# Kernel tuning notes

Measured on AMD Instinct MI355X. Metric: run time of the kernel, lower is better.

The kernel has to match this reference:

```python
import jax, jax.numpy as jnp
import numpy as np

NUM_TOKENS = 8192
CODEBOOK_DIM = 64
BETA = 0.25
DECAY = 0.99
EPS = 1e-05
B, C, H, W = 32, 64, 32, 32


def setup_inputs() -> dict:
    key = jax.random.key(0)
    k1, k2, k3, k4 = jax.random.split(key, 4)
    z = jax.random.normal(k1, (B, C, H, W), dtype=jnp.float32)
    emb = jax.random.normal(k2, (NUM_TOKENS, CODEBOOK_DIM), dtype=jnp.float32)
    ema_w = jax.random.normal(k3, (NUM_TOKENS, CODEBOOK_DIM), dtype=jnp.float32)
    cluster_size = jax.random.uniform(k4, (NUM_TOKENS,), dtype=jnp.float32)
    return {"z": z, "emb": emb, "ema_w": ema_w, "cluster_size": cluster_size}


def reference(z, emb, ema_w, cluster_size):
    # NCHW -> NHWC, flatten to [N, D]
    z_nhwc = jnp.transpose(z, (0, 2, 3, 1))
    z_flat = z_nhwc.reshape(-1, CODEBOOK_DIM)  # [N, D]

    # squared distances: ||z||^2 + ||e||^2 - 2 z e^T  -> [N, K]
    d = (jnp.sum(z_flat * z_flat, axis=1, keepdims=True)
         + jnp.sum(emb * emb, axis=1)
         - 2.0 * jnp.einsum('nd,kd->nk', z_flat, emb))
    idx = jnp.argmin(d, axis=1)  # [N] int

    z_q = emb[idx].reshape(z_nhwc.shape)  # gather + reshape

    # EMA updates (training-mode buffer math); one-hot matmuls expressed as segment sums
    new_cluster = jax.ops.segment_sum(jnp.ones_like(idx, dtype=z.dtype), idx, num_segments=NUM_TOKENS)
    cs = DECAY * cluster_size + (1.0 - DECAY) * new_cluster
    new_ema_w = jax.ops.segment_sum(z_flat, idx, num_segments=NUM_TOKENS)
    ema_w_out = DECAY * ema_w + (1.0 - DECAY) * new_ema_w
    cs_sum = jnp.sum(cs)
    cs_norm = (cs + EPS) / (cs_sum + NUM_TOKENS * EPS)
    emb_out = ema_w_out / cs_norm[:, None]

    # commitment loss uses z_q from the OLD codebook (as in torch code)
    loss = BETA * jnp.mean((jax.lax.stop_gradient(z_q) - z_nhwc) ** 2)

    # straight-through estimator, back to NCHW
    z_q_st = z_nhwc + jax.lax.stop_gradient(z_q - z_nhwc)
    z_q_st = jnp.transpose(z_q_st, (0, 3, 1, 2))
    return z_q_st, loss, idx, cs_norm, ema_w_out, emb_out
```

## Files before the change

### kernel.cpp

```cpp
#include <hip/hip_runtime.h>
#include <float.h>

#define N_TOK   32768
#define DIM     64
#define K_CODES 8192
#define HWSZ    1024
#define CHW     65536
#define NELEM   2097152

typedef short  bf16x8 __attribute__((ext_vector_type(8)));
typedef float  f32x16 __attribute__((ext_vector_type(16)));

static __device__ __forceinline__ unsigned short f2bf(float x) {
    unsigned u = __float_as_uint(x);
    unsigned r = u + 0x7FFFu + ((u >> 16) & 1u);
    return (unsigned short)(r >> 16);
}
static __device__ __forceinline__ float bf2f(unsigned short h) {
    return __uint_as_float(((unsigned)h) << 16);
}

__global__ __launch_bounds__(256) void prep_e(const float* __restrict__ emb,
                                              unsigned short* __restrict__ blob,
                                              float* __restrict__ eng,
                                              unsigned long long* __restrict__ packed,
                                              int* __restrict__ cnt_i,
                                              float* __restrict__ sums) {
    __shared__ float part[512];
    const int gid = blockIdx.x * 256 + threadIdx.x;
    packed[gid] = ~0ull;
    if (gid < K_CODES) cnt_i[gid] = 0;
    if (gid < 2) sums[gid] = 0.f;

    int tile = blockIdx.x;
    #pragma unroll
    for (int u0 = 0; u0 < 2; ++u0) {
        int u = threadIdx.x + u0 * 256;
        int s = u >> 7, h = (u >> 6) & 1, n = u & 63;
        const float* src = emb + (tile * 64 + n) * 64 + s * 16 + h * 8;
        float4 v0 = *(const float4*)src;
        float4 v1 = *(const float4*)(src + 4);
        float x[8] = {v0.x, v0.y, v0.z, v0.w, v1.x, v1.y, v1.z, v1.w};
        unsigned short hi[8], lo[8];
        float ss = 0.f;
        #pragma unroll
        for (int j = 0; j < 8; ++j) {
            hi[j] = f2bf(x[j]);
            lo[j] = f2bf(x[j] - bf2f(hi[j]));
            ss += x[j] * x[j];
        }
        part[u] = ss;
        unsigned short* dhi = blob + (size_t)tile * 8192 + ((s * 2 + 0) * 2 + h) * 512 + n * 8;
        unsigned short* dlo = blob + (size_t)tile * 8192 + ((s * 2 + 1) * 2 + h) * 512 + n * 8;
        uint4 ph, pl;
        ph.x = (unsigned)hi[0] | ((unsigned)hi[1] << 16);
        ph.y = (unsigned)hi[2] | ((unsigned)hi[3] << 16);
        ph.z = (unsigned)hi[4] | ((unsigned)hi[5] << 16);
        ph.w = (unsigned)hi[6] | ((unsigned)hi[7] << 16);
        pl.x = (unsigned)lo[0] | ((unsigned)lo[1] << 16);
        pl.y = (unsigned)lo[2] | ((unsigned)lo[3] << 16);
        pl.z = (unsigned)lo[4] | ((unsigned)lo[5] << 16);
        pl.w = (unsigned)lo[6] | ((unsigned)lo[7] << 16);
        *(uint4*)dhi = ph;
        *(uint4*)dlo = pl;
    }
    __syncthreads();
    if (threadIdx.x < 64) {
        float s = 0.f;
        #pragma unroll
        for (int j = 0; j < 8; ++j) s += part[threadIdx.x + j * 64];
        eng[tile * 64 + threadIdx.x] = s;
    }
}

__global__ __launch_bounds__(256, 3) void vq_argmin(const float* __restrict__ z,
                                                    const unsigned short* __restrict__ blob,
                                                    const float* __restrict__ eng,
                                                    unsigned long long* __restrict__ packed) {
    __shared__ __align__(16) unsigned short zh[64 * 72];
    __shared__ __align__(16) unsigned short zl[64 * 72];
    __shared__ unsigned long long red[64 * 4];

    const int tid  = threadIdx.x;
    const int lane = tid & 63;
    const int wid  = tid >> 6;
    const int l31  = lane & 31, h = lane >> 5;

    const int tb = blockIdx.x & 511;
    const int ks = blockIdx.x >> 9;
    const int n0 = tb * 64;
    const int zbase = (n0 >> 10) * CHW + (n0 & 1023);

    {
        int f4 = tid & 15;
        int c0 = tid >> 4;
        #pragma unroll
        for (int r = 0; r < 4; ++r) {
            int c = c0 * 4 + r;
            float4 v = *(const float4*)(z + zbase + c * HWSZ + f4 * 4);
            float x[4] = {v.x, v.y, v.z, v.w};
            #pragma unroll
            for (int e = 0; e < 4; ++e) {
                int t = f4 * 4 + e;
                float xs = -2.0f * x[e];
                unsigned short hi = f2bf(xs);
                zh[t * 72 + c] = hi;
                zl[t * 72 + c] = f2bf(xs - bf2f(hi));
            }
        }
    }
    __syncthreads();

    bf16x8 T0h[4], T0l[4], T1h[4], T1l[4];
    {
        int r0 = l31;
        int r1 = 32 + l31;
        #pragma unroll
        for (int s = 0; s < 4; ++s) {
            T0h[s] = *(const bf16x8*)(&zh[r0 * 72 + s * 16 + h * 8]);
            T0l[s] = *(const bf16x8*)(&zl[r0 * 72 + s * 16 + h * 8]);
            T1h[s] = *(const bf16x8*)(&zh[r1 * 72 + s * 16 + h * 8]);
            T1l[s] = *(const bf16x8*)(&zl[r1 * 72 + s * 16 + h * 8]);
        }
    }

    float minv0 = FLT_MAX, minv1 = FLT_MAX;
    int   mini0 = 0,       mini1 = 0;

    const int hk0 = ks * 128 + wid, hk1 = ks * 128 + 128;
    for (int hk = hk0; hk < hk1; hk += 4) {
        bf16x8 Eh[4], El[4];
        const unsigned short* base = blob + (size_t)(hk >> 1) * 8192 + ((hk & 1) * 32 + l31) * 8;
        #pragma unroll
        for (int s = 0; s < 4; ++s) {
            Eh[s] = *(const bf16x8*)(base + (4 * s + h) * 512);
            El[s] = *(const bf16x8*)(base + (4 * s + 2 + h) * 512);
        }
        const int cb = (hk >> 1) * 64 + (hk & 1) * 32 + 4 * h;
        const float* ebase = eng + cb;
        float4 e0 = *(const float4*)(ebase);
        float4 e1 = *(const float4*)(ebase + 8);
        float4 e2 = *(const float4*)(ebase + 16);
        float4 e3 = *(const float4*)(ebase + 24);
        f32x16 ac0, ac1;
        ac0[0]  = e0.x; ac0[1]  = e0.y; ac0[2]  = e0.z; ac0[3]  = e0.w;
        ac0[4]  = e1.x; ac0[5]  = e1.y; ac0[6]  = e1.z; ac0[7]  = e1.w;
        ac0[8]  = e2.x; ac0[9]  = e2.y; ac0[10] = e2.z; ac0[11] = e2.w;
        ac0[12] = e3.x; ac0[13] = e3.y; ac0[14] = e3.z; ac0[15] = e3.w;
        ac1 = ac0;
        #pragma unroll
        for (int s = 0; s < 4; ++s) {
            ac0 = __builtin_amdgcn_mfma_f32_32x32x16_bf16(El[s], T0h[s], ac0, 0, 0, 0);
            ac1 = __builtin_amdgcn_mfma_f32_32x32x16_bf16(El[s], T1h[s], ac1, 0, 0, 0);
            ac0 = __builtin_amdgcn_mfma_f32_32x32x16_bf16(Eh[s], T0l[s], ac0, 0, 0, 0);
            ac1 = __builtin_amdgcn_mfma_f32_32x32x16_bf16(Eh[s], T1l[s], ac1, 0, 0, 0);
            ac0 = __builtin_amdgcn_mfma_f32_32x32x16_bf16(Eh[s], T0h[s], ac0, 0, 0, 0);
            ac1 = __builtin_amdgcn_mfma_f32_32x32x16_bf16(Eh[s], T1h[s], ac1, 0, 0, 0);
        }
        #pragma unroll
        for (int r = 0; r < 16; ++r) {
            int code = cb + (r & 3) + 8 * (r >> 2);
            if (ac0[r] < minv0) { minv0 = ac0[r]; mini0 = code; }
            if (ac1[r] < minv1) { minv1 = ac1[r]; mini1 = code; }
        }
    }

    unsigned u0 = __float_as_uint(minv0);
    u0 = (u0 & 0x80000000u) ? ~u0 : (u0 | 0x80000000u);
    unsigned long long k0 = ((unsigned long long)u0 << 32) | (unsigned)mini0;
    unsigned u1 = __float_as_uint(minv1);
    u1 = (u1 & 0x80000000u) ? ~u1 : (u1 | 0x80000000u);
    unsigned long long k1 = ((unsigned long long)u1 << 32) | (unsigned)mini1;
    unsigned long long o0 = __shfl_xor(k0, 32, 64);
    if (o0 < k0) k0 = o0;
    unsigned long long o1 = __shfl_xor(k1, 32, 64);
    if (o1 < k1) k1 = o1;
    if (h == 0) {
        red[l31 * 4 + wid]        = k0;
        red[(32 + l31) * 4 + wid] = k1;
    }
    __syncthreads();
    if (tid < 64) {
        unsigned long long a = red[tid * 4], b = red[tid * 4 + 1];
        unsigned long long c = red[tid * 4 + 2], d = red[tid * 4 + 3];
        unsigned long long m = (b < a) ? b : a;
        if (c < m) m = c;
        if (d < m) m = d;
        atomicMin(&packed[n0 + tid], m);
    }
}

__global__ __launch_bounds__(256) void zq_loss(const float* __restrict__ z,
                                               const float* __restrict__ emb,
                                               const float* __restrict__ ema_w,
                                               const unsigned long long* __restrict__ packed,
                                               float* __restrict__ zq_out,
                                               float* __restrict__ idx_out,
                                               int* __restrict__ idx_i32,
                                               int* __restrict__ cnt_i,
                                               float* __restrict__ loss_sum,
                                               float* __restrict__ z_t,
                                               float* __restrict__ emao_out) {
    const int tid = threadIdx.x;
    const int n0  = blockIdx.x * 64;
    const int t   = tid >> 2, q = tid & 3;
    const int n   = n0 + t;
    const int idx = (int)(packed[n] & 0xFFFFFFFFull);
    if (q == 0) {
        idx_out[n] = (float)idx;
        idx_i32[n] = idx;
        atomicAdd(&cnt_i[idx], 1);
    }
    {
        int g = blockIdx.x * 256 + tid;
        #pragma unroll
        for (int j = 0; j < 4; ++j) {
            int i = g + j * 131072;
            emao_out[i] = 0.99f * ema_w[i];
        }
    }
    const int b = n >> 10, hw = n & 1023;
    const float* er = emb + idx * 64 + q * 16;
    float4 e0 = *(const float4*)er, e1 = *(const float4*)(er + 4);
    float4 e2 = *(const float4*)(er + 8), e3 = *(const float4*)(er + 12);
    float ev[16] = {e0.x, e0.y, e0.z, e0.w, e1.x, e1.y, e1.z, e1.w,
                    e2.x, e2.y, e2.z, e2.w, e3.x, e3.y, e3.z, e3.w};
    float lsum = 0.f;
    #pragma unroll
    for (int j = 0; j < 16; ++j) {
        int c = q * 16 + j;
        float zv = z[b * CHW + c * HWSZ + hw];
        float dd = ev[j] - zv;
        zq_out[b * CHW + c * HWSZ + hw] = zv + dd;
        if (z_t) z_t[n * 64 + c] = zv;
        lsum += dd * dd;
    }
    #pragma unroll
    for (int m = 32; m >= 1; m >>= 1) lsum += __shfl_xor(lsum, m, 64);
    if ((tid & 63) == 0) atomicAdd(loss_sum, lsum);
}

__global__ __launch_bounds__(1024) void scan_cs(const int* __restrict__ cnt_i,
                                                const float* __restrict__ csize,
                                                const float* __restrict__ loss_sum,
                                                int* __restrict__ cursor,
                                                float* __restrict__ csn_out,
                                                float* __restrict__ loss_out) {
    __shared__ int   sc[1024];
    __shared__ float sf[1024];
    const int tid = threadIdx.x;
    int v[8], part = 0;
    float cv[8], fpart = 0.f;
    #pragma unroll
    for (int j = 0; j < 8; ++j) { v[j] = cnt_i[tid * 8 + j]; part += v[j]; }
    #pragma unroll
    for (int j = 0; j < 8; ++j) {
        cv[j] = 0.99f * csize[tid * 8 + j] + 0.01f * (float)v[j];
        fpart += cv[j];
    }
    sc[tid] = part;
    sf[tid] = fpart;
    __syncthreads();
    for (int off = 1; off < 1024; off <<= 1) {
        int add = (tid >= off) ? sc[tid - off] : 0;
        __syncthreads();
        sc[tid] += add;
        __syncthreads();
    }
    int run = sc[tid] - part;
    #pragma unroll
    for (int j = 0; j < 8; ++j) {
        cursor[tid * 8 + j] = run;
        run += v[j];
    }
    for (int off = 512; off >= 1; off >>= 1) {
        if (tid < off) sf[tid] += sf[tid + off];
        __syncthreads();
    }
    float denom = sf[0] + (float)(K_CODES * 1e-5);
    #pragma unroll
    for (int j = 0; j < 8; ++j) csn_out[tid * 8 + j] = (cv[j] + 1e-5f) / denom;
    if (tid == 0) *loss_out = 0.25f * (*loss_sum) * (1.0f / (float)NELEM);
}

__global__ __launch_bounds__(256) void scatter_kernel(const int* __restrict__ idx_i32,
                                                      int* __restrict__ cursor,
                                                      int* __restrict__ tok_of,
                                                      int* __restrict__ code_of) {
    int t = blockIdx.x * 256 + threadIdx.x;
    int k = idx_i32[t];
    int pos = atomicAdd(&cursor[k], 1);
    tok_of[pos] = t;
    code_of[pos] = k;
}

__global__ __launch_bounds__(256) void ema_acc(const float* __restrict__ z,
                                               const float* __restrict__ z_t,
                                               const int* __restrict__ tok_of,
                                               const int* __restrict__ code_of,
                                               float* __restrict__ emao_out) {
    const int wv   = (blockIdx.x * 256 + threadIdx.x) >> 6;
    const int lane = threadIdx.x & 63;
    const int pos0 = wv * 64;
    const int tok  = tok_of[pos0 + lane];
    const int cod  = code_of[pos0 + lane];
    float acc = 0.f;
    #pragma unroll
    for (int g = 0; g < 8; ++g) {
        int tk[8], kk[8];
        #pragma unroll
        for (int j = 0; j < 8; ++j) {
            tk[j] = __shfl(tok, g * 8 + j, 64);
            kk[j] = __shfl(cod, g * 8 + j, 64);
        }
        float v[8];
        if (z_t) {
            #pragma unroll
            for (int j = 0; j < 8; ++j) v[j] = z_t[tk[j] * 64 + lane];
        } else {
            #pragma unroll
            for (int j = 0; j < 8; ++j)
                v[j] = z[(tk[j] >> 10) * CHW + lane * HWSZ + (tk[j] & 1023)];
        }
        int knext = (g < 7) ? __shfl(cod, g * 8 + 8, 64) : -1;
        #pragma unroll
        for (int j = 0; j < 8; ++j) {
            acc += v[j];
            int kn = (j < 7) ? kk[j + 1] : knext;
            if (kn != kk[j]) {
                atomicAdd(&emao_out[kk[j] * 64 + lane], 0.01f * acc);
                acc = 0.f;
            }
        }
    }
}

__global__ __launch_bounds__(256) void final_div(const float* __restrict__ emao_out,
                                                 const float* __restrict__ csn_out,
                                                 float* __restrict__ embo_out) {
    int g = blockIdx.x * 256 + threadIdx.x;
    embo_out[g] = emao_out[g] / csn_out[g >> 6];
}

extern "C" void kernel_launch(void* const* d_in, const int* in_sizes, int n_in,
                              void* d_out, int out_size, void* d_ws, size_t ws_size,
                              hipStream_t stream) {
    (void)in_sizes; (void)n_in; (void)out_size;
    const float* z     = (const float*)d_in[0];
    const float* emb   = (const float*)d_in[1];
    const float* ema_w = (const float*)d_in[2];
    const float* csize = (const float*)d_in[3];

    float* out      = (float*)d_out;
    float* zq_out   = out;
    float* loss_out = out + 2097152;
    float* idx_out  = out + 2097153;
    float* csn_out  = out + 2129921;
    float* emao_out = out + 2138113;
    float* embo_out = out + 2662401;

    char* wsb = (char*)d_ws;
    unsigned short*     blob    = (unsigned short*)(wsb);
    float*              eng     = (float*)(wsb + 2097152);
    unsigned long long* packed  = (unsigned long long*)(wsb + 2129920);
    int*                code_of = (int*)(wsb + 2129920);
    int*                idx_i32 = (int*)(wsb + 2392064);
    int*                cnt_i   = (int*)(wsb + 2523136);
    float*              sums    = (float*)(wsb + 2555904);
    int*                cursor  = (int*)(wsb + 2555920);
    int*                tok_of  = (int*)(wsb + 2588688);
    const size_t zt_off = 2719760;
    float* z_t = (ws_size >= zt_off + (size_t)NELEM * 4) ? (float*)(wsb + zt_off) : nullptr;

    prep_e<<<128, 256, 0, stream>>>(emb, blob, eng, packed, cnt_i, sums);
    vq_argmin<<<1024, 256, 0, stream>>>(z, blob, eng, packed);
    zq_loss<<<N_TOK / 64, 256, 0, stream>>>(z, emb, ema_w, packed, zq_out, idx_out,
                                            idx_i32, cnt_i, sums + 1, z_t, emao_out);
    scan_cs<<<1, 1024, 0, stream>>>(cnt_i, csize, sums + 1, cursor, csn_out, loss_out);
    scatter_kernel<<<N_TOK / 256, 256, 0, stream>>>(idx_i32, cursor, tok_of, code_of);
    ema_acc<<<128, 256, 0, stream>>>(z, z_t, tok_of, code_of, emao_out);
    final_div<<<K_CODES * DIM / 256, 256, 0, stream>>>(emao_out, csn_out, embo_out);
}
```

Baseline: 239.3 us.

## Software-pipeline codebook loads in the argmin MFMA loop and raise wave priority

Restructures the distance/argmin loop so the next iteration's bf16 codebook fragments and code-norm values are fetched from global memory while the current iteration's MFMAs run. The aim is to hide global load latency behind the matrix work instead of stalling at the top of each iteration. It also raises wave priority around the MFMA block with s_setprio, and keeps the code index as a wave-uniform scalar, adding the per-lane offset once after the loop. The extra live fragment registers can lower occupancy. The final prefetch reads one tile past the wave's range, which may touch memory beyond the end of the buffer for the last slice.

```diff
diff --git a/kernel.cpp b/kernel.cpp
--- a/kernel.cpp
+++ b/kernel.cpp
@@ -124,30 +124,40 @@
         }
     }
 
+    const int hk0 = ks * 128 + wid;
+    const unsigned short* bp = blob + (size_t)(hk0 >> 1) * 8192 + ((hk0 & 1) * 32 + l31) * 8;
+    const float* ep = eng + (hk0 >> 1) * 64 + (hk0 & 1) * 32 + 4 * h;
+    int scode = __builtin_amdgcn_readfirstlane((hk0 >> 1) * 64 + (hk0 & 1) * 32);
+
+    bf16x8 Eh[4], El[4];
+    #pragma unroll
+    for (int s = 0; s < 4; ++s) {
+        Eh[s] = *(const bf16x8*)(bp + (4 * s + h) * 512);
+        El[s] = *(const bf16x8*)(bp + (4 * s + 2 + h) * 512);
+    }
+    float4 g0 = *(const float4*)(ep);
+    float4 g1 = *(const float4*)(ep + 8);
+    float4 g2 = *(const float4*)(ep + 16);
+    float4 g3 = *(const float4*)(ep + 24);
+
     float minv0 = FLT_MAX, minv1 = FLT_MAX;
     int   mini0 = 0,       mini1 = 0;
 
-    const int hk0 = ks * 128 + wid, hk1 = ks * 128 + 128;
-    for (int hk = hk0; hk < hk1; hk += 4) {
-        bf16x8 Eh[4], El[4];
-        const unsigned short* base = blob + (size_t)(hk >> 1) * 8192 + ((hk & 1) * 32 + l31) * 8;
-        #pragma unroll
-        for (int s = 0; s < 4; ++s) {
-            Eh[s] = *(const bf16x8*)(base + (4 * s + h) * 512);
-            El[s] = *(const bf16x8*)(base + (4 * s + 2 + h) * 512);
-        }
-        const int cb = (hk >> 1) * 64 + (hk & 1) * 32 + 4 * h;
-        const float* ebase = eng + cb;
-        float4 e0 = *(const float4*)(ebase);
-        float4 e1 = *(const float4*)(ebase + 8);
-        float4 e2 = *(const float4*)(ebase + 16);
-        float4 e3 = *(const float4*)(ebase + 24);
+    for (int i = 0; i < 32; ++i) {
         f32x16 ac0, ac1;
-        ac0[0]  = e0.x; ac0[1]  = e0.y; ac0[2]  = e0.z; ac0[3]  = e0.w;
-        ac0[4]  = e1.x; ac0[5]  = e1.y; ac0[6]  = e1.z; ac0[7]  = e1.w;
-        ac0[8]  = e2.x; ac0[9]  = e2.y; ac0[10] = e2.z; ac0[11] = e2.w;
-        ac0[12] = e3.x; ac0[13] = e3.y; ac0[14] = e3.z; ac0[15] = e3.w;
+        ac0[0]  = g0.x; ac0[1]  = g0.y; ac0[2]  = g0.z; ac0[3]  = g0.w;
+        ac0[4]  = g1.x; ac0[5]  = g1.y; ac0[6]  = g1.z; ac0[7]  = g1.w;
+        ac0[8]  = g2.x; ac0[9]  = g2.y; ac0[10] = g2.z; ac0[11] = g2.w;
+        ac0[12] = g3.x; ac0[13] = g3.y; ac0[14] = g3.z; ac0[15] = g3.w;
         ac1 = ac0;
+
+        ep += 128;
+        g0 = *(const float4*)(ep);
+        g1 = *(const float4*)(ep + 8);
+        g2 = *(const float4*)(ep + 16);
+        g3 = *(const float4*)(ep + 24);
+
+        __builtin_amdgcn_s_setprio(1);
         #pragma unroll
         for (int s = 0; s < 4; ++s) {
             ac0 = __builtin_amdgcn_mfma_f32_32x32x16_bf16(El[s], T0h[s], ac0, 0, 0, 0);
@@ -157,13 +167,25 @@
             ac0 = __builtin_amdgcn_mfma_f32_32x32x16_bf16(Eh[s], T0h[s], ac0, 0, 0, 0);
             ac1 = __builtin_amdgcn_mfma_f32_32x32x16_bf16(Eh[s], T1h[s], ac1, 0, 0, 0);
         }
+        __builtin_amdgcn_s_setprio(0);
+
+        bp += 2 * 8192;
+        #pragma unroll
+        for (int s = 0; s < 4; ++s) {
+            Eh[s] = *(const bf16x8*)(bp + (4 * s + h) * 512);
+            El[s] = *(const bf16x8*)(bp + (4 * s + 2 + h) * 512);
+        }
+
         #pragma unroll
         for (int r = 0; r < 16; ++r) {
-            int code = cb + (r & 3) + 8 * (r >> 2);
+            int code = scode + ((r & 3) + 8 * (r >> 2));
             if (ac0[r] < minv0) { minv0 = ac0[r]; mini0 = code; }
             if (ac1[r] < minv1) { minv1 = ac1[r]; mini1 = code; }
         }
-    }
+        scode += 128;
+    }
+    mini0 += 4 * h;
+    mini1 += 4 * h;
 
     unsigned u0 = __float_as_uint(minv0);
     u0 = (u0 & 0x80000000u) ? ~u0 : (u0 | 0x80000000u);
```

New measurement: 224.0 us. 1.07x faster.
